# Optimization experiments

Hardware: AMD Instinct MI355X
Metric: run time of the kernel (lower is better)

The kernel has to match this reference:

```python
import jax, jax.numpy as jnp
import numpy as np

# Hyper-params from init_kwargs
H, DM, DA, DP, M, T = 8, 512, 256, 128, 32, 4096
DK, DAh, DPh = DM // H, DA // H, DP // H   # 64, 32, 16
B, K_STEPS = 8, 2048
S = T + K_STEPS          # length of x = memory + x_pre
EPS = 1e-12

def _l2n(x):
    # F.normalize(p=2, dim=-1)
    return x / jnp.maximum(jnp.linalg.norm(x, axis=-1, keepdims=True), EPS)

def setup_inputs() -> dict:
    key = jax.random.key(0)
    ks = jax.random.split(key, 28)
    n = lambda i, s, sc=0.05: jax.random.normal(ks[i], s, jnp.float32) * sc
    return {
        "memory": jax.random.normal(ks[0], (B, S - 1, DM), jnp.float32),
        "x_pre":  jax.random.normal(ks[1], (B, 1, DM), jnp.float32),
        "aux":    jax.random.normal(ks[2], (B, S, DA), jnp.float32),
        "pos":    jax.random.normal(ks[3], (B, S, DP), jnp.float32),
        "Wq": n(4, (H, DK, DM)), "bq": n(5, (H, DK)),
        "Wk": n(6, (H, DK, DM)), "bk": n(7, (H, DK)),
        "Wv": n(8, (H, DK, DM)), "bv": n(9, (H, DK)),
        "Wqa": n(10, (H, DAh, DA)), "bqa": n(11, (H, DAh)),
        "Wka": n(12, (H, DAh, DA)), "bka": n(13, (H, DAh)),
        "Wqp": n(14, (H, DPh, DP)), "bqp": n(15, (H, DPh)),
        "Wkp": n(16, (H, DPh, DP)), "bkp": n(17, (H, DPh)),
        "W_ih": n(18, (3 * DK, DM)), "W_hh": n(19, (3 * DK, DK)),
        "b_ih": n(20, (3 * DK,)), "b_hh": n(21, (3 * DK,)),
        "WO": n(22, (DM, DM)), "bO": n(23, (DM,)),
        "w": n(24, (1, 1), 1.0), "w_a": n(25, (1, 1), 1.0), "w_p": n(26, (1, 1), 1.0),
        "G": (jax.random.uniform(ks[27], (DK, DK)) < 0.5).astype(jnp.int32),
        "k": K_STEPS,
    }

def _forward(memory, x_pre, aux, pos, Wq, bq, Wk, bk, Wv, bv, Wqa, bqa, Wka, bka,
             Wqp, bqp, Wkp, bkp, W_ih, W_hh, b_ih, b_hh, WO, bO, w, w_a, w_p, G, k):
    b = memory.shape[0]
    x = jnp.concatenate([memory, x_pre], axis=1)           # [B, S, DM]
    s = x.shape[1]
    Wn = k + T - M + 1                                     # attention window length
    g = G.astype(x.dtype)
    mask_h = jnp.tile(g, (1, H))[None]                     # [1, DK, DM] per-head SparseLinear mask

    # per-head Q/K node projections (SparseLinear), L2-normalized
    Q = _l2n(jnp.einsum('bsd,hkd->bhsk', x, Wq * mask_h) + bq[None, :, None, :])
    K = _l2n(jnp.einsum('bsd,hkd->bhsk', x, Wk * mask_h) + bk[None, :, None, :])

    # tn_transform_pre: for each position p, mean over the M-step window of Qv[m].K[p+m]
    Qv = Q[:, :, -M:, :]                                   # [B,H,M,DK]
    D = jnp.einsum('bhmd,bhsd->bhms', Qv, K)               # [B,H,M,S]
    p_idx = jnp.arange(Wn)[None, :] + jnp.arange(M)[:, None]   # [M,Wn]
    band = D[:, :, jnp.arange(M)[:, None], p_idx]          # [B,H,M,Wn] band-diagonal gather
    tn = band.mean(axis=2)                                 # [B,H,Wn]

    # aux / pos similarities: only the last query row survives the slice in the source
    QA = _l2n(jnp.einsum('bsa,hca->bhsc', aux, Wqa) + bqa[None, :, None, :])
    KA = _l2n(jnp.einsum('bsa,hca->bhsc', aux, Wka) + bka[None, :, None, :])
    dot2 = jnp.einsum('bhc,bhsc->bhs', QA[:, :, -1, :], KA[:, :, aux.shape[1] - Wn:, :])
    QP = _l2n(jnp.einsum('bsp,hcp->bhsc', pos, Wqp) + bqp[None, :, None, :])
    KP = _l2n(jnp.einsum('bsp,hcp->bhsc', pos, Wkp) + bkp[None, :, None, :])
    dot3 = jnp.einsum('bhc,bhsc->bhs', QP[:, :, -1, :], KP[:, :, pos.shape[1] - Wn:, :])

    attn = jax.nn.softmax(w[0, 0] * tn + w_a[0, 0] * dot2 + w_p[0, 0] * dot3, axis=-1)  # [B,H,Wn]

    # value projection over the history window, weighted by attn[..., :-1]
    xv = x[:, s - Wn:s - 1, :]                             # [B, Wn-1, DM]
    V = jnp.einsum('bsd,hkd->bhsk', xv, Wv * mask_h) + bv[None, :, None, :]
    hist = jnp.einsum('bhw,bhwd->bhd', attn[:, :, :-1], V) # [B,H,DK]

    # sequential GRU over the recent M-1 steps (shared across heads)
    recent = jnp.swapaxes(x[:, -M:-1, :], 0, 1)            # [M-1, B, DM]
    def cell(hprev, xt):
        gi = xt @ W_ih.T + b_ih
        gh = hprev @ W_hh.T + b_hh
        ir, iz, inn = jnp.split(gi, 3, axis=-1)
        hr, hz, hn = jnp.split(gh, 3, axis=-1)
        r = jax.nn.sigmoid(ir + hr)
        z = jax.nn.sigmoid(iz + hz)
        nst = jnp.tanh(inn + r * hn)
        return (1.0 - z) * nst + z * hprev, None
    res, _ = jax.lax.scan(cell, jnp.zeros((b, DK), x.dtype), recent)  # [B, DK]

    # concat per-head deltas (deta[:, :, 1:] just drops the initial zeros column)
    deta = (hist + attn[:, :, -1:] * res[:, None, :]).reshape(b, H * DK)   # [B, DM]
    mask_o = jnp.tile(g, (H, H))                           # [DM, DM] for W_O
    out = x_pre + (deta @ (WO * mask_o).T + bO)[:, None, :]
    return out

def reference(memory, x_pre, aux, pos, Wq, bq, Wk, bk, Wv, bv, Wqa, bqa, Wka, bka,
              Wqp, bqp, Wkp, bkp, W_ih, W_hh, b_ih, b_hh, WO, bO, w, w_a, w_p, G, k):
    return _forward(memory, x_pre, aux, pos, Wq, bq, Wk, bk, Wv, bv, Wqa, bqa, Wka,
                    bka, Wqp, bqp, Wkp, bkp, W_ih, W_hh, b_ih, b_hh, WO, bO,
                    w, w_a, w_p, G, k)
```

## Files before the change

### kernel.cpp

```cpp
#include <hip/hip_runtime.h>
#include <math.h>

#define BB   8
#define S    6144
#define SM1  6143
#define DM   512
#define H    8
#define DK   64
#define M    32
#define WN   6113
#define DA   256
#define DAh  32
#define DP   128
#define DPh  16
#define EPSN 1e-12f

#define WS_WKT    0
#define WS_WKAT   262144
#define WS_WKPT   327680
#define WS_QHAT   344064
#define WS_QAHAT  475136
#define WS_QPHAT  477184
#define WS_LOGITS 478208
#define WS_XBAR   869440
#define WS_ALAST  902208
#define WS_RES    902272
#define WS_GI     902784
#define WS_WQM    950400
#define WS_XBF    1212544
#define N_LOGITS  391232
#define N_XBAR    32768

typedef __attribute__((ext_vector_type(8))) short short8;
typedef __attribute__((ext_vector_type(4))) float f32x4;

__device__ inline unsigned short f2bf(float f) {
    union { float f; unsigned u; } v; v.f = f;
    unsigned r = v.u + 0x7fffu + ((v.u >> 16) & 1u);
    return (unsigned short)(r >> 16);
}
__device__ inline float bf2f(unsigned short u) {
    union { unsigned u; float f; } v; v.u = ((unsigned)u) << 16; return v.f;
}

union S8U { short8 v; unsigned short e[8]; };

__global__ void prep_weights(const float* __restrict__ Wk, const float* __restrict__ Wka,
                             const float* __restrict__ Wkp, const float* __restrict__ Wq,
                             const int* __restrict__ G,
                             unsigned short* __restrict__ wkb,
                             unsigned short* __restrict__ wkab,
                             unsigned short* __restrict__ wkpb,
                             float* __restrict__ wqm)
{
    int idx = blockIdx.x * 256 + threadIdx.x;
    if (idx < H*DM*DK) {
        int k = idx & 63; int d = (idx >> 6) & 511; int h = idx >> 15;
        float v = Wk[(size_t)(h*DK + k)*DM + d] * (float)G[k*DK + (d & 63)];
        wkb[(size_t)h*DM*DK + (((d >> 3)*DK + k) << 3) + (d & 7)] = f2bf(v);
    }
    int i2 = idx - H*DM*DK;
    if (i2 >= 0 && i2 < H*DA*DAh) {
        int h = i2 >> 13; int r = i2 & 8191;
        int j = r & 7; int f = r >> 3;
        int c = f & 31; int a = (f >> 5)*8 + j;
        wkab[i2] = f2bf(Wka[(size_t)(h*DAh + c)*DA + a]);
    }
    int i3 = idx - H*DM*DK - H*DA*DAh;
    if (i3 >= 0 && i3 < H*DP*DPh) {
        int h = i3 >> 11; int r = i3 & 2047;
        int j = r & 7; int f = r >> 3;
        int c = f & 15; int p = (f >> 4)*8 + j;
        wkpb[i3] = f2bf(Wkp[(size_t)(h*DPh + c)*DP + p]);
    }
    int i4 = idx - H*DM*DK - H*DA*DAh - H*DP*DPh;
    if (i4 >= 0 && i4 < H*DK*DM) {
        int d = i4 & 511; int k = (i4 >> 9) & 63;
        wqm[i4] = Wq[i4] * (float)G[k*DK + (d & 63)];
    }
}

__global__ __launch_bounds__(256) void xcast_k(
    const float* __restrict__ memory, const float* __restrict__ x_pre,
    unsigned short* __restrict__ xbf)
{
    size_t e = ((size_t)blockIdx.x*256 + threadIdx.x)*8;
    int b = (int)(e / ((size_t)S*DM));
    size_t r = e - (size_t)b*S*DM;
    int t = (int)(r >> 9);
    int d = (int)(r & 511);
    const float* src = (t < SM1) ? memory + ((size_t)b*SM1 + t)*DM + d
                                 : x_pre + (size_t)b*DM + d;
    float4 v0 = *(const float4*)src, v1 = *(const float4*)(src + 4);
    S8U t8;
    t8.e[0]=f2bf(v0.x); t8.e[1]=f2bf(v0.y); t8.e[2]=f2bf(v0.z); t8.e[3]=f2bf(v0.w);
    t8.e[4]=f2bf(v1.x); t8.e[5]=f2bf(v1.y); t8.e[6]=f2bf(v1.z); t8.e[7]=f2bf(v1.w);
    *(short8*)(xbf + e) = t8.v;
}

__global__ __launch_bounds__(256) void qhat_k2(
    const float* __restrict__ memory, const float* __restrict__ x_pre,
    const float* __restrict__ wqm, const float* __restrict__ bq,
    float* __restrict__ qhat)
{
    int bx = blockIdx.x;
    int mp = bx & 15;
    int h  = (bx >> 4) & 7;
    int b  = bx >> 7;
    int tid = threadIdx.x;
    int k = tid & 63, dq = tid >> 6;

    int m0 = mp*2;
    int t0 = S - M + m0, t1 = t0 + 1;
    const float* x0 = ((t0 < SM1) ? memory + ((size_t)b*SM1 + t0)*DM
                                  : x_pre + (size_t)b*DM) + dq*128;
    const float* x1 = ((t1 < SM1) ? memory + ((size_t)b*SM1 + t1)*DM
                                  : x_pre + (size_t)b*DM) + dq*128;
    const float* wr = wqm + (size_t)(h*DK + k)*DM + dq*128;

    float s0 = 0.f, s1 = 0.f;
    #pragma unroll 8
    for (int d = 0; d < 128; d += 4) {
        float4 w4 = *(const float4*)(wr + d);
        float4 a4 = *(const float4*)(x0 + d);
        float4 b4 = *(const float4*)(x1 + d);
        s0 += w4.x*a4.x + w4.y*a4.y + w4.z*a4.z + w4.w*a4.w;
        s1 += w4.x*b4.x + w4.y*b4.y + w4.z*b4.z + w4.w*b4.w;
    }

    __shared__ float part[2][4][64];
    part[0][dq][k] = s0;
    part[1][dq][k] = s1;
    __syncthreads();

    if (tid < 128) {
        int mi = tid >> 6;
        int kk = tid & 63;
        float q = part[mi][0][kk] + part[mi][1][kk] + part[mi][2][kk] + part[mi][3][kk]
                + bq[h*DK + kk];
        float ss = q*q;
        #pragma unroll
        for (int d2 = 1; d2 <= 32; d2 <<= 1) ss += __shfl_xor(ss, d2);
        qhat[((size_t)(b*H + h)*M + (m0 + mi))*DK + kk] = q / fmaxf(sqrtf(ss), EPSN);
    }
}

__global__ __launch_bounds__(256) void qaqp_k(
    const float* __restrict__ aux, const float* __restrict__ pos,
    const float* __restrict__ Wqa, const float* __restrict__ bqa,
    const float* __restrict__ Wqp, const float* __restrict__ bqp,
    float* __restrict__ qahat, float* __restrict__ qphat)
{
    int bh = blockIdx.x; int b = bh >> 3, h = bh & 7;
    int tid = threadIdx.x;
    __shared__ float pa[32][8];
    __shared__ float pp[16][16];

    {
        int c = tid & 31, ch = tid >> 5;
        const float* ar = aux + ((size_t)b*S + (S-1))*DA + ch*32;
        const float* wv = Wqa + (size_t)(h*DAh + c)*DA + ch*32;
        float s = 0.f;
        #pragma unroll
        for (int a = 0; a < 32; a += 4) {
            float4 a4 = *(const float4*)(ar + a);
            float4 w4 = *(const float4*)(wv + a);
            s += a4.x*w4.x + a4.y*w4.y + a4.z*w4.z + a4.w*w4.w;
        }
        pa[c][ch] = s;
    }
    {
        int c = tid & 15, ch = tid >> 4;
        const float* pr = pos + ((size_t)b*S + (S-1))*DP + ch*8;
        const float* wv = Wqp + (size_t)(h*DPh + c)*DP + ch*8;
        float4 a4 = *(const float4*)(pr);
        float4 w4 = *(const float4*)(wv);
        float4 a5 = *(const float4*)(pr + 4);
        float4 w5 = *(const float4*)(wv + 4);
        pp[c][ch] = a4.x*w4.x + a4.y*w4.y + a4.z*w4.z + a4.w*w4.w
                  + a5.x*w5.x + a5.y*w5.y + a5.z*w5.z + a5.w*w5.w;
    }
    __syncthreads();

    if (tid < 32) {
        float q = bqa[h*DAh + tid];
        #pragma unroll
        for (int ch = 0; ch < 8; ++ch) q += pa[tid][ch];
        float ss = q*q;
        #pragma unroll
        for (int d2 = 1; d2 <= 16; d2 <<= 1) ss += __shfl_xor(ss, d2);
        qahat[(size_t)bh*DAh + tid] = q / fmaxf(sqrtf(ss), EPSN);
    } else if (tid >= 64 && tid < 80) {
        int c = tid - 64;
        float q = bqp[h*DPh + c];
        #pragma unroll
        for (int ch = 0; ch < 16; ++ch) q += pp[c][ch];
        float ss = q*q;
        #pragma unroll
        for (int d2 = 1; d2 <= 8; d2 <<= 1) ss += __shfl_xor(ss, d2);
        qphat[(size_t)bh*DPh + c] = q / fmaxf(sqrtf(ss), EPSN);
    }
}

__global__ __launch_bounds__(256, 4) void kproj_mfma3(
    const unsigned short* __restrict__ xbf, const unsigned short* __restrict__ wkb,
    const float* __restrict__ bk, const float* __restrict__ qhat,
    const float* __restrict__ wscal, float* __restrict__ logits)
{
    int bx = blockIdx.x;
    int tile = bx % 96, h = (bx / 96) & 7, b = bx / (96*8);
    int t0 = tile * 64;
    int tid = threadIdx.x;
    int wave = tid >> 6, lane = tid & 63;
    int quad = lane >> 4, l16 = lane & 15;

    __shared__ unsigned short Qs[M][72];
    __shared__ unsigned short Kb[64][72];
    __shared__ float tnloc[95];

    {
        const float* qsrc = qhat + (size_t)(b*H + h)*M*DK;
        int i = tid * 8;
        float4 a0 = *(const float4*)(qsrc + i);
        float4 a1 = *(const float4*)(qsrc + i + 4);
        S8U t8;
        t8.e[0]=f2bf(a0.x); t8.e[1]=f2bf(a0.y); t8.e[2]=f2bf(a0.z); t8.e[3]=f2bf(a0.w);
        t8.e[4]=f2bf(a1.x); t8.e[5]=f2bf(a1.y); t8.e[6]=f2bf(a1.z); t8.e[7]=f2bf(a1.w);
        *(short8*)&Qs[i >> 6][i & 63] = t8.v;
    }
    if (tid < 95) tnloc[tid] = 0.f;

    f32x4 acc[4];
    #pragma unroll
    for (int nt = 0; nt < 4; ++nt) acc[nt] = (f32x4){0.f,0.f,0.f,0.f};

    const unsigned short* xrow = xbf + ((size_t)b*S + t0 + wave*16 + l16)*DM;
    const unsigned short* wh = wkb + (size_t)h*DM*DK;

    #pragma unroll
    for (int ch = 0; ch < 4; ++ch) {
        #pragma unroll
        for (int ks = 0; ks < 4; ++ks) {
            short8 a = *(const short8*)(xrow + ch*128 + ks*32 + quad*8);
            #pragma unroll
            for (int nt = 0; nt < 4; ++nt) {
                short8 bf = *(const short8*)(wh + (((ch*16 + ks*4 + quad)*DK) + nt*16 + l16)*8);
                acc[nt] = __builtin_amdgcn_mfma_f32_16x16x32_bf16(a, bf, acc[nt], 0, 0, 0);
            }
        }
    }

    {
        float vv[4][4];
        float ss[4] = {0.f, 0.f, 0.f, 0.f};
        #pragma unroll
        for (int nt = 0; nt < 4; ++nt) {
            float bkv = bk[h*DK + nt*16 + l16];
            #pragma unroll
            for (int reg = 0; reg < 4; ++reg) {
                float v = acc[nt][reg] + bkv;
                vv[nt][reg] = v;
                ss[reg] += v*v;
            }
        }
        #pragma unroll
        for (int d2 = 1; d2 <= 8; d2 <<= 1)
            #pragma unroll
            for (int reg = 0; reg < 4; ++reg) ss[reg] += __shfl_xor(ss[reg], d2);
        #pragma unroll
        for (int reg = 0; reg < 4; ++reg) {
            float inv = 1.f / fmaxf(sqrtf(ss[reg]), EPSN);
            #pragma unroll
            for (int nt = 0; nt < 4; ++nt)
                Kb[wave*16 + quad*4 + reg][nt*16 + l16] = f2bf(vv[nt][reg] * inv);
        }
    }
    __syncthreads();

    {
        int mtile = wave & 1;
        int thalf = (wave >> 1) * 32;
        f32x4 acc2[2];
        acc2[0] = (f32x4){0.f,0.f,0.f,0.f};
        acc2[1] = (f32x4){0.f,0.f,0.f,0.f};
        #pragma unroll
        for (int ks = 0; ks < 2; ++ks) {
            short8 a = *(const short8*)&Qs[mtile*16 + l16][ks*32 + quad*8];
            #pragma unroll
            for (int nt = 0; nt < 2; ++nt) {
                short8 kf = *(const short8*)&Kb[thalf + nt*16 + l16][ks*32 + quad*8];
                acc2[nt] = __builtin_amdgcn_mfma_f32_16x16x32_bf16(a, kf, acc2[nt], 0, 0, 0);
            }
        }
        int m0 = mtile*16 + quad*4;
        #pragma unroll
        for (int nt = 0; nt < 2; ++nt) {
            int tl = thalf + nt*16 + l16;
            #pragma unroll
            for (int reg = 0; reg < 4; ++reg) {
                int mm = m0 + reg;
                int j = t0 + tl - mm;
                if (j >= 0 && j < WN)
                    atomicAdd(&tnloc[tl - mm + 31], acc2[nt][reg]);
            }
        }
    }
    __syncthreads();
    if (tid < 95) {
        int j = t0 + tid - 31;
        if (j >= 0 && j < WN)
            atomicAdd(&logits[(size_t)(b*H + h)*WN + j], wscal[0]*(1.f/32.f)*tnloc[tid]);
    }
}

__global__ __launch_bounds__(256, 2) void ka_proj_mfma(
    const float* __restrict__ aux, const unsigned short* __restrict__ wkab,
    const float* __restrict__ bka, const float* __restrict__ qahat,
    const float* __restrict__ wa, float* __restrict__ logits)
{
    int tile = blockIdx.x % 96;
    int b    = blockIdx.x / 96;
    int j0   = tile * 64;
    int tid  = threadIdx.x;
    int wave = tid >> 6, lane = tid & 63;
    int quad = lane >> 4, l16 = lane & 15;

    __shared__ unsigned short Xa[32*520];

    {
        int r = tid >> 2, seg = tid & 3;
        int j = j0 + r; if (j > WN-1) j = WN-1;
        const float* ar = aux + ((size_t)b*S + (31 + j))*DA + seg*64;
        int tt = r >> 4, lo = r & 15;
        #pragma unroll
        for (int g = 0; g < 8; ++g) {
            float4 v0 = *(const float4*)(ar + g*8);
            float4 v1 = *(const float4*)(ar + g*8 + 4);
            int d0 = seg*64 + g*8;
            int ks = d0 >> 5, qd = (d0 >> 3) & 3;
            S8U t8;
            t8.e[0]=f2bf(v0.x); t8.e[1]=f2bf(v0.y); t8.e[2]=f2bf(v0.z); t8.e[3]=f2bf(v0.w);
            t8.e[4]=f2bf(v1.x); t8.e[5]=f2bf(v1.y); t8.e[6]=f2bf(v1.z); t8.e[7]=f2bf(v1.w);
            *(short8*)&Xa[(tt*8 + ks)*520 + (qd*16 + lo)*8] = t8.v;
        }
    }
    __syncthreads();

    float wav = wa[0];
    for (int h = 0; h < H; ++h) {
        const unsigned short* wsrc = wkab + (size_t)h*DA*DAh;
        f32x4 acc[2];
        acc[0] = (f32x4){0.f,0.f,0.f,0.f};
        acc[1] = (f32x4){0.f,0.f,0.f,0.f};
        #pragma unroll
        for (int ks = 0; ks < 8; ++ks) {
            short8 a = *(const short8*)&Xa[(wave*8 + ks)*520 + lane*8];
            #pragma unroll
            for (int nt = 0; nt < 2; ++nt) {
                short8 bf = *(const short8*)(wsrc + (size_t)(((ks*4 + quad)*32) + nt*16 + l16)*8);
                acc[nt] = __builtin_amdgcn_mfma_f32_16x16x32_bf16(a, bf, acc[nt], 0, 0, 0);
            }
        }
        float bk0 = bka[h*DAh + l16], bk1 = bka[h*DAh + 16 + l16];
        float q0 = qahat[(size_t)(b*H + h)*DAh + l16];
        float q1 = qahat[(size_t)(b*H + h)*DAh + 16 + l16];
        #pragma unroll
        for (int reg = 0; reg < 4; ++reg) {
            float v0 = acc[0][reg] + bk0;
            float v1 = acc[1][reg] + bk1;
            float ss = v0*v0 + v1*v1;
            float dp = v0*q0 + v1*q1;
            #pragma unroll
            for (int d2 = 1; d2 <= 8; d2 <<= 1) {
                ss += __shfl_xor(ss, d2);
                dp += __shfl_xor(dp, d2);
            }
            if (l16 == 0) {
                int j = j0 + wave*16 + quad*4 + reg;
                if (j < WN)
                    logits[(size_t)(b*H + h)*WN + j] += wav * dp / fmaxf(sqrtf(ss), EPSN);
            }
        }
    }
}

__global__ __launch_bounds__(256, 2) void kp_proj_mfma(
    const float* __restrict__ pos, const unsigned short* __restrict__ wkpb,
    const float* __restrict__ bkp, const float* __restrict__ qphat,
    const float* __restrict__ wp, float* __restrict__ logits)
{
    int tile = blockIdx.x % 96;
    int b    = blockIdx.x / 96;
    int j0   = tile * 64;
    int tid  = threadIdx.x;
    int wave = tid >> 6, lane = tid & 63;
    int quad = lane >> 4, l16 = lane & 15;

    __shared__ unsigned short Xp[16*520];

    {
        int r = tid >> 2, seg = tid & 3;
        int j = j0 + r; if (j > WN-1) j = WN-1;
        const float* pr = pos + ((size_t)b*S + (31 + j))*DP + seg*32;
        int tt = r >> 4, lo = r & 15;
        #pragma unroll
        for (int g = 0; g < 4; ++g) {
            float4 v0 = *(const float4*)(pr + g*8);
            float4 v1 = *(const float4*)(pr + g*8 + 4);
            int d0 = seg*32 + g*8;
            int ks = d0 >> 5, qd = (d0 >> 3) & 3;
            S8U t8;
            t8.e[0]=f2bf(v0.x); t8.e[1]=f2bf(v0.y); t8.e[2]=f2bf(v0.z); t8.e[3]=f2bf(v0.w);
            t8.e[4]=f2bf(v1.x); t8.e[5]=f2bf(v1.y); t8.e[6]=f2bf(v1.z); t8.e[7]=f2bf(v1.w);
            *(short8*)&Xp[(tt*4 + ks)*520 + (qd*16 + lo)*8] = t8.v;
        }
    }
    __syncthreads();

    float wpv = wp[0];
    for (int h = 0; h < H; ++h) {
        const unsigned short* wsrc = wkpb + (size_t)h*DP*DPh;
        f32x4 acc = (f32x4){0.f,0.f,0.f,0.f};
        #pragma unroll
        for (int ks = 0; ks < 4; ++ks) {
            short8 a = *(const short8*)&Xp[(wave*4 + ks)*520 + lane*8];
            short8 bf = *(const short8*)(wsrc + (size_t)(((ks*4 + quad)*16) + l16)*8);
            acc = __builtin_amdgcn_mfma_f32_16x16x32_bf16(a, bf, acc, 0, 0, 0);
        }
        float bk0 = bkp[h*DPh + l16];
        float q0 = qphat[(size_t)(b*H + h)*DPh + l16];
        #pragma unroll
        for (int reg = 0; reg < 4; ++reg) {
            float v = acc[reg] + bk0;
            float ss = v*v;
            float dp = v*q0;
            #pragma unroll
            for (int d2 = 1; d2 <= 8; d2 <<= 1) {
                ss += __shfl_xor(ss, d2);
                dp += __shfl_xor(dp, d2);
            }
            if (l16 == 0) {
                int j = j0 + wave*16 + quad*4 + reg;
                if (j < WN)
                    logits[(size_t)(b*H + h)*WN + j] += wpv * dp / fmaxf(sqrtf(ss), EPSN);
            }
        }
    }
}

__global__ __launch_bounds__(256, 2) void kproj_band_mfma2(
    const float* __restrict__ memory, const float* __restrict__ x_pre,
    const unsigned short* __restrict__ wkb, const float* __restrict__ bk,
    const float* __restrict__ qhat, const float* __restrict__ wscal,
    float* __restrict__ logits)
{
    int bx = blockIdx.x;
    int hp = bx & 3, b = (bx >> 2) & 7, tile = bx >> 5;
    int t0 = tile * 128;
    int tid = threadIdx.x;
    int wave = tid >> 6, lane = tid & 63;
    int quad = lane >> 4, l16 = lane & 15;

    __shared__ unsigned short Xf[32*520];
    __shared__ unsigned short Wf[16*520];
    __shared__ unsigned short Kb[128][72];
    __shared__ unsigned short Qs[M][72];
    __shared__ float tnloc[159];

    if (tid < 159) tnloc[tid] = 0.f;
    {
        int h = hp*2;
        const float* qsrc = qhat + (size_t)(b*H + h)*M*DK;
        int i = tid * 8;
        float4 a0 = *(const float4*)(qsrc + i);
        float4 a1 = *(const float4*)(qsrc + i + 4);
        S8U t8;
        t8.e[0]=f2bf(a0.x); t8.e[1]=f2bf(a0.y); t8.e[2]=f2bf(a0.z); t8.e[3]=f2bf(a0.w);
        t8.e[4]=f2bf(a1.x); t8.e[5]=f2bf(a1.y); t8.e[6]=f2bf(a1.z); t8.e[7]=f2bf(a1.w);
        *(short8*)&Qs[i >> 6][i & 63] = t8.v;
    }

    f32x4 acc[2][2][4];
    #pragma unroll
    for (int hi = 0; hi < 2; ++hi)
        #pragma unroll
        for (int mt = 0; mt < 2; ++mt)
            #pragma unroll
            for (int nt = 0; nt < 4; ++nt) acc[hi][mt][nt] = (f32x4){0.f,0.f,0.f,0.f};

    for (int ch = 0; ch < 4; ++ch) {
        __syncthreads();
        {
            int r = tid >> 1, half = tid & 1;
            int t = t0 + r;
            const float* xr = ((t < SM1) ? (memory + ((size_t)b*SM1 + t)*DM)
                                         : (x_pre + (size_t)b*DM)) + ch*128 + half*64;
            int tt = r >> 4, lo = r & 15;
            #pragma unroll
            for (int g = 0; g < 8; ++g) {
                float4 v0 = *(const float4*)(xr + g*8);
// ... 96 lines not shown
        }
        __syncthreads();
        {
            f32x4 acc2[2][2];
            #pragma unroll
            for (int mt = 0; mt < 2; ++mt)
                #pragma unroll
                for (int nt = 0; nt < 2; ++nt) acc2[mt][nt] = (f32x4){0.f,0.f,0.f,0.f};
            #pragma unroll
            for (int ks = 0; ks < 2; ++ks) {
                short8 qa0 = *(const short8*)&Qs[l16     ][ks*32 + quad*8];
                short8 qa1 = *(const short8*)&Qs[16 + l16][ks*32 + quad*8];
                #pragma unroll
                for (int nt = 0; nt < 2; ++nt) {
                    short8 kf = *(const short8*)&Kb[wave*32 + nt*16 + l16][ks*32 + quad*8];
                    acc2[0][nt] = __builtin_amdgcn_mfma_f32_16x16x32_bf16(qa0, kf, acc2[0][nt], 0, 0, 0);
                    acc2[1][nt] = __builtin_amdgcn_mfma_f32_16x16x32_bf16(qa1, kf, acc2[1][nt], 0, 0, 0);
                }
            }
            #pragma unroll
            for (int mt = 0; mt < 2; ++mt)
                #pragma unroll
                for (int nt = 0; nt < 2; ++nt) {
                    int tcol = wave*32 + nt*16 + l16;
                    #pragma unroll
                    for (int reg = 0; reg < 4; ++reg) {
                        int m = mt*16 + quad*4 + reg;
                        int j = t0 + tcol - m;
                        if (j >= 0 && j < WN)
                            atomicAdd(&tnloc[tcol - m + 31], acc2[mt][nt][reg]);
                    }
                }
        }
        __syncthreads();
        if (tid < 159) {
            int j = t0 + tid - 31;
            if (j >= 0 && j < WN)
                atomicAdd(&logits[(size_t)(b*H + h)*WN + j], wom * tnloc[tid]);
            tnloc[tid] = 0.f;
        }
        if (hi == 0) {
            const float* qsrc = qhat + (size_t)(b*H + h + 1)*M*DK;
            int i = tid * 8;
            float4 a0 = *(const float4*)(qsrc + i);
            float4 a1 = *(const float4*)(qsrc + i + 4);
            S8U t8;
            t8.e[0]=f2bf(a0.x); t8.e[1]=f2bf(a0.y); t8.e[2]=f2bf(a0.z); t8.e[3]=f2bf(a0.w);
            t8.e[4]=f2bf(a1.x); t8.e[5]=f2bf(a1.y); t8.e[6]=f2bf(a1.z); t8.e[7]=f2bf(a1.w);
            *(short8*)&Qs[i >> 6][i & 63] = t8.v;
        }
    }
}

__global__ __launch_bounds__(256) void softmax_k(float* __restrict__ logits,
                                                 float* __restrict__ alast)
{
    int bh = blockIdx.x;
    float* L = logits + (size_t)bh*WN;
    __shared__ float red[256];
    int tid = threadIdx.x;
    float mx = -1e30f;
    for (int j = tid; j < WN; j += 256) mx = fmaxf(mx, L[j]);
    red[tid] = mx; __syncthreads();
    for (int s2 = 128; s2 > 0; s2 >>= 1) {
        if (tid < s2) red[tid] = fmaxf(red[tid], red[tid+s2]);
        __syncthreads();
    }
    mx = red[0]; __syncthreads();
    float sm = 0.f;
    for (int j = tid; j < WN; j += 256) sm += expf(L[j] - mx);
    red[tid] = sm; __syncthreads();
    for (int s2 = 128; s2 > 0; s2 >>= 1) {
        if (tid < s2) red[tid] += red[tid+s2];
        __syncthreads();
    }
    float inv = 1.f / red[0];
    for (int j = tid; j < WN; j += 256) {
        float a = expf(L[j] - mx) * inv;
        L[j] = a;
        if (j == WN-1) alast[bh] = a;
    }
}

#define JC 191
__global__ __launch_bounds__(256) void xbar_bf_k(
    const unsigned short* __restrict__ xbf, const float* __restrict__ attn,
    float* __restrict__ xbar)
{
    int chunk = blockIdx.x & 31;
    int b = blockIdx.x >> 5;
    int j0 = chunk * JC;
    __shared__ float al[H][JC];
    int tid = threadIdx.x;
    for (int i = tid; i < H*JC; i += 256) {
        int hh = i / JC, jj = i - hh*JC;
        al[hh][jj] = attn[(size_t)(b*H + hh)*WN + j0 + jj];
    }
    __syncthreads();
    int d0 = tid * 2;
    const unsigned* p = (const unsigned*)(xbf + ((size_t)b*S + 31 + j0)*DM + d0);
    float acc[H][2];
    #pragma unroll
    for (int hh = 0; hh < H; ++hh) { acc[hh][0] = 0.f; acc[hh][1] = 0.f; }
    for (int jj = 0; jj < JC; ++jj) {
        unsigned u = p[(size_t)jj*(DM/2)];
        float x0 = bf2f((unsigned short)(u & 0xffff));
        float x1 = bf2f((unsigned short)(u >> 16));
        #pragma unroll
        for (int hh = 0; hh < H; ++hh) {
            float a = al[hh][jj];
            acc[hh][0] += a * x0;
            acc[hh][1] += a * x1;
        }
    }
    #pragma unroll
    for (int hh = 0; hh < H; ++hh) {
        atomicAdd(&xbar[(size_t)(b*H+hh)*DM + d0],     acc[hh][0]);
        atomicAdd(&xbar[(size_t)(b*H+hh)*DM + d0 + 1], acc[hh][1]);
    }
}

__global__ __launch_bounds__(256) void xbar_k(
    const float* __restrict__ memory, const float* __restrict__ attn,
    float* __restrict__ xbar)
{
    int chunk = blockIdx.x & 31;
    int b = blockIdx.x >> 5;
    int j0 = chunk * JC;
    __shared__ float al[H][JC];
    int tid = threadIdx.x;
    for (int i = tid; i < H*JC; i += 256) {
        int hh = i / JC, jj = i - hh*JC;
        al[hh][jj] = attn[(size_t)(b*H + hh)*WN + j0 + jj];
    }
    __syncthreads();
    int d0 = tid * 2;
    float acc[H][2];
    #pragma unroll
    for (int hh = 0; hh < H; ++hh) { acc[hh][0] = 0.f; acc[hh][1] = 0.f; }
    for (int jj = 0; jj < JC; ++jj) {
        int t = 31 + j0 + jj;
        const float2 xv = *(const float2*)(memory + ((size_t)b*SM1 + t)*DM + d0);
        #pragma unroll
        for (int hh = 0; hh < H; ++hh) {
            float a = al[hh][jj];
            acc[hh][0] += a * xv.x;
            acc[hh][1] += a * xv.y;
        }
    }
    #pragma unroll
    for (int hh = 0; hh < H; ++hh) {
        atomicAdd(&xbar[(size_t)(b*H+hh)*DM + d0],     acc[hh][0]);
        atomicAdd(&xbar[(size_t)(b*H+hh)*DM + d0 + 1], acc[hh][1]);
    }
}

__global__ __launch_bounds__(192) void gi_k(
    const float* __restrict__ memory, const float* __restrict__ W_ih,
    const float* __restrict__ b_ih, float* __restrict__ gi_all)
{
    int t = blockIdx.x >> 3;
    int b = blockIdx.x & 7;
    int c = threadIdx.x;
    const float* xr = memory + ((size_t)b*SM1 + (S - M) + t)*DM;
    const float* wr = W_ih + (size_t)c*DM;
    float s = b_ih[c];
    for (int d = 0; d < DM; d += 4) {
        float4 x4 = *(const float4*)(xr + d);
        float4 w4 = *(const float4*)(wr + d);
        s += x4.x*w4.x + x4.y*w4.y + x4.z*w4.z + x4.w*w4.w;
    }
    gi_all[((size_t)t*BB + b)*192 + c] = s;
}

__global__ __launch_bounds__(512) void gru_scan(
    const float* __restrict__ gi_all, const float* __restrict__ W_hh,
    const float* __restrict__ b_hh, float* __restrict__ res)
{
    int b = threadIdx.x >> 6;
    int l = threadIdx.x & 63;

    float w0[64], w1[64], w2[64];
    {
        const float* r0p = W_hh + (size_t)l*DK;
        const float* r1p = W_hh + (size_t)(64 + l)*DK;
        const float* r2p = W_hh + (size_t)(128 + l)*DK;
        #pragma unroll
        for (int i = 0; i < 16; ++i) {
            float4 a = *(const float4*)(r0p + i*4);
            w0[i*4]=a.x; w0[i*4+1]=a.y; w0[i*4+2]=a.z; w0[i*4+3]=a.w;
            float4 c = *(const float4*)(r1p + i*4);
            w1[i*4]=c.x; w1[i*4+1]=c.y; w1[i*4+2]=c.z; w1[i*4+3]=c.w;
            float4 e = *(const float4*)(r2p + i*4);
            w2[i*4]=e.x; w2[i*4+1]=e.y; w2[i*4+2]=e.z; w2[i*4+3]=e.w;
        }
    }
    float bh0 = b_hh[l], bh1 = b_hh[64 + l], bh2 = b_hh[128 + l];

    float h = 0.f;
    const float* g0 = gi_all + (size_t)b*192;
    float gr = g0[l], gz = g0[64 + l], gn = g0[128 + l];

    #pragma unroll 1
    for (int t = 0; t < 31; ++t) {
        float a0 = bh0, a1 = bh1, a2 = bh2;
        #pragma unroll
        for (int k = 0; k < 64; ++k) {
            float hk = __int_as_float(__builtin_amdgcn_readlane(__float_as_int(h), k));
            a0 += hk * w0[k];
            a1 += hk * w1[k];
            a2 += hk * w2[k];
        }
        float ngr = 0.f, ngz = 0.f, ngn = 0.f;
        if (t < 30) {
            const float* g2 = gi_all + ((size_t)(t+1)*BB + b)*192;
            ngr = g2[l]; ngz = g2[64 + l]; ngn = g2[128 + l];
        }
        float r = 1.f / (1.f + expf(-(gr + a0)));
        float z = 1.f / (1.f + expf(-(gz + a1)));
        float n = tanhf(gn + r * a2);
        h = (1.f - z)*n + z*h;
        gr = ngr; gz = ngz; gn = ngn;
    }
    res[b*DK + l] = h;
}
// ... 45 lines not shown
                              hipStream_t stream)
{
    const float* memory = (const float*)d_in[0];
    const float* x_pre  = (const float*)d_in[1];
    const float* aux    = (const float*)d_in[2];
    const float* pos    = (const float*)d_in[3];
    const float* Wq  = (const float*)d_in[4];
    const float* bq  = (const float*)d_in[5];
    const float* Wk  = (const float*)d_in[6];
    const float* bk  = (const float*)d_in[7];
    const float* Wv  = (const float*)d_in[8];
    const float* bv  = (const float*)d_in[9];
    const float* Wqa = (const float*)d_in[10];
    const float* bqa = (const float*)d_in[11];
    const float* Wka = (const float*)d_in[12];
    const float* bka = (const float*)d_in[13];
    const float* Wqp = (const float*)d_in[14];
    const float* bqp = (const float*)d_in[15];
    const float* Wkp = (const float*)d_in[16];
    const float* bkp = (const float*)d_in[17];
    const float* W_ih = (const float*)d_in[18];
    const float* W_hh = (const float*)d_in[19];
    const float* b_ih = (const float*)d_in[20];
    const float* b_hh = (const float*)d_in[21];
    const float* WO  = (const float*)d_in[22];
    const float* bO  = (const float*)d_in[23];
    const float* w   = (const float*)d_in[24];
    const float* w_a = (const float*)d_in[25];
    const float* w_p = (const float*)d_in[26];
    const int*   G   = (const int*)d_in[27];
    (void)in_sizes; (void)n_in; (void)out_size;

    float* ws = (float*)d_ws;
    unsigned short* wkb  = (unsigned short*)(ws + WS_WKT);
    unsigned short* wkab = (unsigned short*)(ws + WS_WKAT);
    unsigned short* wkpb = (unsigned short*)(ws + WS_WKPT);
    float* qhat   = ws + WS_QHAT;
    float* qahat  = ws + WS_QAHAT;
    float* qphat  = ws + WS_QPHAT;
    float* logits = ws + WS_LOGITS;
    float* xbar   = ws + WS_XBAR;
    float* alast  = ws + WS_ALAST;
    float* resb   = ws + WS_RES;
    float* gi_all = ws + WS_GI;
    float* wqm    = ws + WS_WQM;
    unsigned short* xbf = (unsigned short*)(ws + WS_XBF);
    float* outp   = (float*)d_out;

    const size_t need = ((size_t)WS_XBF + 12582912) * 4;
    const bool big = (ws_size >= need);

    hipMemsetAsync(logits, 0, (size_t)(N_LOGITS + N_XBAR)*sizeof(float), stream);

    prep_weights<<<(H*DM*DK + H*DA*DAh + H*DP*DPh + H*DK*DM + 255)/256, 256, 0, stream>>>(
        Wk, Wka, Wkp, Wq, G, wkb, wkab, wkpb, wqm);

    if (big)
        xcast_k<<<12288, 256, 0, stream>>>(memory, x_pre, xbf);

    gi_k<<<31*BB, 192, 0, stream>>>(memory, W_ih, b_ih, gi_all);
    gru_scan<<<1, 512, 0, stream>>>(gi_all, W_hh, b_hh, resb);

    qhat_k2<<<BB*H*16, 256, 0, stream>>>(memory, x_pre, wqm, bq, qhat);
    qaqp_k<<<BB*H, 256, 0, stream>>>(aux, pos, Wqa, bqa, Wqp, bqp, qahat, qphat);

    if (big)
        kproj_mfma3<<<96*8*BB, 256, 0, stream>>>(xbf, wkb, bk, qhat, w, logits);
    else
        kproj_band_mfma2<<<48*BB*4, 256, 0, stream>>>(memory, x_pre, wkb, bk, qhat,
                                                      w, logits);

    ka_proj_mfma<<<BB*96, 256, 0, stream>>>(aux, wkab, bka, qahat, w_a, logits);
    kp_proj_mfma<<<BB*96, 256, 0, stream>>>(pos, wkpb, bkp, qphat, w_p, logits);

    softmax_k<<<BB*H, 256, 0, stream>>>(logits, alast);

    if (big)
        xbar_bf_k<<<BB*32, 256, 0, stream>>>(xbf, logits, xbar);
    else
        xbar_k<<<BB*32, 256, 0, stream>>>(memory, logits, xbar);

    final_k<<<BB, 512, 0, stream>>>(x_pre, xbar, Wv, bv, WO, bO, alast, resb, G, outp);
}
```

Baseline: 614.0 us.

## Fuse prelude and projection kernels; widen softmax and xbar parallelism

Merges the weight prep, GRU input projection and bf16 cast into one prelude launch, and merges the K, aux and pos logit projections into one launch whose blocks are interleaved and dispatched by block index. The ka/kp contributions to the logits switch from plain += to atomicAdd because they now run concurrently with the K projection. Softmax moves to 1024 threads per block and the xbar reduction uses twice as many chunks. The goals are fewer launch gaps, overlap between independent projections and more parallelism in the short tail kernels, at the cost of extra atomics and a larger shared-memory footprint for the fused kernel.

```diff
diff --git a/kernel.cpp b/kernel.cpp
--- a/kernel.cpp
+++ b/kernel.cpp
@@ -45,57 +45,80 @@
 
 union S8U { short8 v; unsigned short e[8]; };
 
-__global__ void prep_weights(const float* __restrict__ Wk, const float* __restrict__ Wka,
-                             const float* __restrict__ Wkp, const float* __restrict__ Wq,
-                             const int* __restrict__ G,
-                             unsigned short* __restrict__ wkb,
-                             unsigned short* __restrict__ wkab,
-                             unsigned short* __restrict__ wkpb,
-                             float* __restrict__ wqm)
-{
-    int idx = blockIdx.x * 256 + threadIdx.x;
-    if (idx < H*DM*DK) {
-        int k = idx & 63; int d = (idx >> 6) & 511; int h = idx >> 15;
-        float v = Wk[(size_t)(h*DK + k)*DM + d] * (float)G[k*DK + (d & 63)];
-        wkb[(size_t)h*DM*DK + (((d >> 3)*DK + k) << 3) + (d & 7)] = f2bf(v);
-    }
-    int i2 = idx - H*DM*DK;
-    if (i2 >= 0 && i2 < H*DA*DAh) {
-        int h = i2 >> 13; int r = i2 & 8191;
-        int j = r & 7; int f = r >> 3;
-        int c = f & 31; int a = (f >> 5)*8 + j;
-        wkab[i2] = f2bf(Wka[(size_t)(h*DAh + c)*DA + a]);
-    }
-    int i3 = idx - H*DM*DK - H*DA*DAh;
-    if (i3 >= 0 && i3 < H*DP*DPh) {
-        int h = i3 >> 11; int r = i3 & 2047;
-        int j = r & 7; int f = r >> 3;
-        int c = f & 15; int p = (f >> 4)*8 + j;
-        wkpb[i3] = f2bf(Wkp[(size_t)(h*DPh + c)*DP + p]);
-    }
-    int i4 = idx - H*DM*DK - H*DA*DAh - H*DP*DPh;
-    if (i4 >= 0 && i4 < H*DK*DM) {
-        int d = i4 & 511; int k = (i4 >> 9) & 63;
-        wqm[i4] = Wq[i4] * (float)G[k*DK + (d & 63)];
-    }
-}
-
-__global__ __launch_bounds__(256) void xcast_k(
+#define PREP_NB 2368
+#define GI_NB   248
+#define XCAST_NB 12288
+
+__global__ __launch_bounds__(256) void prelude_k(
+    const float* __restrict__ Wk, const float* __restrict__ Wka,
+    const float* __restrict__ Wkp, const float* __restrict__ Wq,
+    const int* __restrict__ G,
+    unsigned short* __restrict__ wkb, unsigned short* __restrict__ wkab,
+    unsigned short* __restrict__ wkpb, float* __restrict__ wqm,
     const float* __restrict__ memory, const float* __restrict__ x_pre,
-    unsigned short* __restrict__ xbf)
-{
-    size_t e = ((size_t)blockIdx.x*256 + threadIdx.x)*8;
-    int b = (int)(e / ((size_t)S*DM));
-    size_t r = e - (size_t)b*S*DM;
-    int t = (int)(r >> 9);
-    int d = (int)(r & 511);
-    const float* src = (t < SM1) ? memory + ((size_t)b*SM1 + t)*DM + d
-                                 : x_pre + (size_t)b*DM + d;
-    float4 v0 = *(const float4*)src, v1 = *(const float4*)(src + 4);
-    S8U t8;
-    t8.e[0]=f2bf(v0.x); t8.e[1]=f2bf(v0.y); t8.e[2]=f2bf(v0.z); t8.e[3]=f2bf(v0.w);
-    t8.e[4]=f2bf(v1.x); t8.e[5]=f2bf(v1.y); t8.e[6]=f2bf(v1.z); t8.e[7]=f2bf(v1.w);
-    *(short8*)(xbf + e) = t8.v;
+    const float* __restrict__ W_ih, const float* __restrict__ b_ih,
+    float* __restrict__ gi_all, unsigned short* __restrict__ xbf)
+{
+    int bx = blockIdx.x, tid = threadIdx.x;
+
+    if (bx < PREP_NB) {
+        int idx = bx * 256 + tid;
+        if (idx < H*DM*DK) {
+            int k = idx & 63; int d = (idx >> 6) & 511; int h = idx >> 15;
+            float v = Wk[(size_t)(h*DK + k)*DM + d] * (float)G[k*DK + (d & 63)];
+            wkb[(size_t)h*DM*DK + (((d >> 3)*DK + k) << 3) + (d & 7)] = f2bf(v);
+        }
+        int i2 = idx - H*DM*DK;
+        if (i2 >= 0 && i2 < H*DA*DAh) {
+            int h = i2 >> 13; int r = i2 & 8191;
+            int j = r & 7; int f = r >> 3;
+            int c = f & 31; int a = (f >> 5)*8 + j;
+            wkab[i2] = f2bf(Wka[(size_t)(h*DAh + c)*DA + a]);
+        }
+        int i3 = idx - H*DM*DK - H*DA*DAh;
+        if (i3 >= 0 && i3 < H*DP*DPh) {
+            int h = i3 >> 11; int r = i3 & 2047;
+            int j = r & 7; int f = r >> 3;
+            int c = f & 15; int p = (f >> 4)*8 + j;
+            wkpb[i3] = f2bf(Wkp[(size_t)(h*DPh + c)*DP + p]);
+        }
+        int i4 = idx - H*DM*DK - H*DA*DAh - H*DP*DPh;
+        if (i4 >= 0 && i4 < H*DK*DM) {
+            int d = i4 & 511; int k = (i4 >> 9) & 63;
+            wqm[i4] = Wq[i4] * (float)G[k*DK + (d & 63)];
+        }
+        return;
+    }
+    if (bx < PREP_NB + GI_NB) {
+        if (tid < 192) {
+            int gx = bx - PREP_NB;
+            int t = gx >> 3, b = gx & 7, c = tid;
+            const float* xr = memory + ((size_t)b*SM1 + (S - M) + t)*DM;
+            const float* wr = W_ih + (size_t)c*DM;
+            float s = b_ih[c];
+            for (int d = 0; d < DM; d += 4) {
+                float4 x4 = *(const float4*)(xr + d);
+                float4 w4 = *(const float4*)(wr + d);
+                s += x4.x*w4.x + x4.y*w4.y + x4.z*w4.z + x4.w*w4.w;
+            }
+            gi_all[((size_t)t*BB + b)*192 + c] = s;
+        }
+        return;
+    }
+    {
+        size_t e = ((size_t)(bx - PREP_NB - GI_NB)*256 + tid)*8;
+        int b = (int)(e / ((size_t)S*DM));
+        size_t r = e - (size_t)b*S*DM;
+        int t = (int)(r >> 9);
+        int d = (int)(r & 511);
+        const float* src = (t < SM1) ? memory + ((size_t)b*SM1 + t)*DM + d
+                                     : x_pre + (size_t)b*DM + d;
+        float4 v0 = *(const float4*)src, v1 = *(const float4*)(src + 4);
+        S8U t8;
+        t8.e[0]=f2bf(v0.x); t8.e[1]=f2bf(v0.y); t8.e[2]=f2bf(v0.z); t8.e[3]=f2bf(v0.w);
+        t8.e[4]=f2bf(v1.x); t8.e[5]=f2bf(v1.y); t8.e[6]=f2bf(v1.z); t8.e[7]=f2bf(v1.w);
+        *(short8*)(xbf + e) = t8.v;
+    }
 }
 
 __global__ __launch_bounds__(256) void qhat_k2(
@@ -202,21 +225,22 @@
     }
 }
 
-__global__ __launch_bounds__(256, 4) void kproj_mfma3(
+#define SMEM_BYTES 33280
+
+__device__ __forceinline__ void kproj3_body(int bxx, int tid, unsigned char* smemraw,
     const unsigned short* __restrict__ xbf, const unsigned short* __restrict__ wkb,
     const float* __restrict__ bk, const float* __restrict__ qhat,
     const float* __restrict__ wscal, float* __restrict__ logits)
 {
-    int bx = blockIdx.x;
-    int tile = bx % 96, h = (bx / 96) & 7, b = bx / (96*8);
+    int tile = bxx % 96, h = (bxx / 96) & 7, b = bxx / (96*8);
     int t0 = tile * 64;
-    int tid = threadIdx.x;
     int wave = tid >> 6, lane = tid & 63;
     int quad = lane >> 4, l16 = lane & 15;
 
-    __shared__ unsigned short Qs[M][72];
-    __shared__ unsigned short Kb[64][72];
-    __shared__ float tnloc[95];
+    typedef unsigned short row72[72];
+    row72* Qs = (row72*)smemraw;
+    row72* Kb = (row72*)(smemraw + 32*72*2);
+    float* tnloc = (float*)(smemraw + 96*72*2);
 
     {
         const float* qsrc = qhat + (size_t)(b*H + h)*M*DK;
@@ -313,19 +337,18 @@
     }
 }
 
-__global__ __launch_bounds__(256, 2) void ka_proj_mfma(
+__device__ __forceinline__ void ka_body(int g, int tid, unsigned char* smemraw,
     const float* __restrict__ aux, const unsigned short* __restrict__ wkab,
     const float* __restrict__ bka, const float* __restrict__ qahat,
     const float* __restrict__ wa, float* __restrict__ logits)
 {
-    int tile = blockIdx.x % 96;
-    int b    = blockIdx.x / 96;
+    int tile = g % 96;
+    int b    = g / 96;
     int j0   = tile * 64;
-    int tid  = threadIdx.x;
     int wave = tid >> 6, lane = tid & 63;
     int quad = lane >> 4, l16 = lane & 15;
 
-    __shared__ unsigned short Xa[32*520];
+    unsigned short* Xa = (unsigned short*)smemraw;
 
     {
         int r = tid >> 2, seg = tid & 3;
@@ -333,10 +356,10 @@
         const float* ar = aux + ((size_t)b*S + (31 + j))*DA + seg*64;
         int tt = r >> 4, lo = r & 15;
         #pragma unroll
-        for (int g = 0; g < 8; ++g) {
-            float4 v0 = *(const float4*)(ar + g*8);
-            float4 v1 = *(const float4*)(ar + g*8 + 4);
-            int d0 = seg*64 + g*8;
+        for (int gg = 0; gg < 8; ++gg) {
+            float4 v0 = *(const float4*)(ar + gg*8);
+            float4 v1 = *(const float4*)(ar + gg*8 + 4);
+            int d0 = seg*64 + gg*8;
             int ks = d0 >> 5, qd = (d0 >> 3) & 3;
             S8U t8;
             t8.e[0]=f2bf(v0.x); t8.e[1]=f2bf(v0.y); t8.e[2]=f2bf(v0.z); t8.e[3]=f2bf(v0.w);
@@ -378,25 +401,25 @@
             if (l16 == 0) {
                 int j = j0 + wave*16 + quad*4 + reg;
                 if (j < WN)
-                    logits[(size_t)(b*H + h)*WN + j] += wav * dp / fmaxf(sqrtf(ss), EPSN);
-            }
-        }
-    }
-}
-
-__global__ __launch_bounds__(256, 2) void kp_proj_mfma(
+                    atomicAdd(&logits[(size_t)(b*H + h)*WN + j],
+                              wav * dp / fmaxf(sqrtf(ss), EPSN));
+            }
+        }
+    }
+}
+
+__device__ __forceinline__ void kp_body(int g, int tid, unsigned char* smemraw,
     const float* __restrict__ pos, const unsigned short* __restrict__ wkpb,
     const float* __restrict__ bkp, const float* __restrict__ qphat,
     const float* __restrict__ wp, float* __restrict__ logits)
 {
-    int tile = blockIdx.x % 96;
-    int b    = blockIdx.x / 96;
+    int tile = g % 96;
+    int b    = g / 96;
     int j0   = tile * 64;
-    int tid  = threadIdx.x;
     int wave = tid >> 6, lane = tid & 63;
     int quad = lane >> 4, l16 = lane & 15;
 
-    __shared__ unsigned short Xp[16*520];
+    unsigned short* Xp = (unsigned short*)smemraw;
 
     {
         int r = tid >> 2, seg = tid & 3;
@@ -404,10 +427,10 @@
         const float* pr = pos + ((size_t)b*S + (31 + j))*DP + seg*32;
         int tt = r >> 4, lo = r & 15;
         #pragma unroll
-        for (int g = 0; g < 4; ++g) {
-            float4 v0 = *(const float4*)(pr + g*8);
-            float4 v1 = *(const float4*)(pr + g*8 + 4);
-            int d0 = seg*32 + g*8;
+        for (int gg = 0; gg < 4; ++gg) {
+            float4 v0 = *(const float4*)(pr + gg*8);
+            float4 v1 = *(const float4*)(pr + gg*8 + 4);
+            int d0 = seg*32 + gg*8;
             int ks = d0 >> 5, qd = (d0 >> 3) & 3;
             S8U t8;
             t8.e[0]=f2bf(v0.x); t8.e[1]=f2bf(v0.y); t8.e[2]=f2bf(v0.z); t8.e[3]=f2bf(v0.w);
@@ -442,10 +465,52 @@
             if (l16 == 0) {
                 int j = j0 + wave*16 + quad*4 + reg;
                 if (j < WN)
-                    logits[(size_t)(b*H + h)*WN + j] += wpv * dp / fmaxf(sqrtf(ss), EPSN);
-            }
-        }
-    }
+                    atomicAdd(&logits[(size_t)(b*H + h)*WN + j],
+                              wpv * dp / fmaxf(sqrtf(ss), EPSN));
+            }
+        }
+    }
+}
+
+__global__ __launch_bounds__(256, 4) void proj_fused_k(
+    const unsigned short* __restrict__ xbf, const unsigned short* __restrict__ wkb,
+    const float* __restrict__ bk, const float* __restrict__ qhat,
+    const float* __restrict__ w,
+    const float* __restrict__ aux, const unsigned short* __restrict__ wkab,
+    const float* __restrict__ bka, const float* __restrict__ qahat,
+    const float* __restrict__ wa,
+    const float* __restrict__ pos, const unsigned short* __restrict__ wkpb,
+    const float* __restrict__ bkp, const float* __restrict__ qphat,
+    const float* __restrict__ wp,
+    float* __restrict__ logits)
+{
+    __shared__ __align__(16) unsigned char smemraw[SMEM_BYTES];
+    int bx = blockIdx.x;
+    int g = bx / 10, r = bx - g*10;
+    int tid = threadIdx.x;
+    if (r < 8)
+        kproj3_body(g*8 + r, tid, smemraw, xbf, wkb, bk, qhat, w, logits);
+    else if (r == 8)
+        ka_body(g, tid, smemraw, aux, wkab, bka, qahat, wa, logits);
+    else
+        kp_body(g, tid, smemraw, pos, wkpb, bkp, qphat, wp, logits);
+}
+
+__global__ __launch_bounds__(256, 2) void ka_only_k(
+    const float* __restrict__ aux, const unsigned short* __restrict__ wkab,
+    const float* __restrict__ bka, const float* __restrict__ qahat,
+    const float* __restrict__ wa, float* __restrict__ logits)
+{
+    __shared__ __align__(16) unsigned char smemraw[SMEM_BYTES];
+    ka_body(blockIdx.x, threadIdx.x, smemraw, aux, wkab, bka, qahat, wa, logits);
+}
+__global__ __launch_bounds__(256, 2) void kp_only_k(
+    const float* __restrict__ pos, const unsigned short* __restrict__ wkpb,
+    const float* __restrict__ bkp, const float* __restrict__ qphat,
+    const float* __restrict__ wp, float* __restrict__ logits)
+{
+    __shared__ __align__(16) unsigned char smemraw[SMEM_BYTES];
+    kp_body(blockIdx.x, threadIdx.x, smemraw, pos, wkpb, bkp, qphat, wp, logits);
 }
 
 __global__ __launch_bounds__(256, 2) void kproj_band_mfma2(
@@ -648,39 +713,79 @@
     }
 }
 
-__global__ __launch_bounds__(256) void softmax_k(float* __restrict__ logits,
-                                                 float* __restrict__ alast)
+__global__ __launch_bounds__(1024) void softmax_k(float* __restrict__ logits,
+                                                  float* __restrict__ alast)
 {
     int bh = blockIdx.x;
     float* L = logits + (size_t)bh*WN;
-    __shared__ float red[256];
+    __shared__ float red[1024];
     int tid = threadIdx.x;
     float mx = -1e30f;
-    for (int j = tid; j < WN; j += 256) mx = fmaxf(mx, L[j]);
+    for (int j = tid; j < WN; j += 1024) mx = fmaxf(mx, L[j]);
     red[tid] = mx; __syncthreads();
-    for (int s2 = 128; s2 > 0; s2 >>= 1) {
+    for (int s2 = 512; s2 > 0; s2 >>= 1) {
         if (tid < s2) red[tid] = fmaxf(red[tid], red[tid+s2]);
         __syncthreads();
     }
     mx = red[0]; __syncthreads();
     float sm = 0.f;
-    for (int j = tid; j < WN; j += 256) sm += expf(L[j] - mx);
+    for (int j = tid; j < WN; j += 1024) sm += expf(L[j] - mx);
     red[tid] = sm; __syncthreads();
-    for (int s2 = 128; s2 > 0; s2 >>= 1) {
+    for (int s2 = 512; s2 > 0; s2 >>= 1) {
         if (tid < s2) red[tid] += red[tid+s2];
         __syncthreads();
     }
     float inv = 1.f / red[0];
-    for (int j = tid; j < WN; j += 256) {
+    for (int j = tid; j < WN; j += 1024) {
         float a = expf(L[j] - mx) * inv;
         L[j] = a;
         if (j == WN-1) alast[bh] = a;
     }
 }
 
-#define JC 191
+#define JC2 96
 __global__ __launch_bounds__(256) void xbar_bf_k(
     const unsigned short* __restrict__ xbf, const float* __restrict__ attn,
+    float* __restrict__ xbar)
+{
+    int chunk = blockIdx.x & 63;
+    int b = blockIdx.x >> 6;
+    int j0 = chunk * JC2;
+    int lim = (WN-1) - j0; if (lim > JC2) lim = JC2; if (lim < 0) lim = 0;
+    __shared__ float al[H][JC2];
+    int tid = threadIdx.x;
+    for (int i = tid; i < H*JC2; i += 256) {
+        int hh = i / JC2, jj = i - hh*JC2;
+        al[hh][jj] = (jj < lim) ? attn[(size_t)(b*H + hh)*WN + j0 + jj] : 0.f;
+    }
+    __syncthreads();
+    int d0 = tid * 2;
+    const unsigned* p = (const unsigned*)(xbf + ((size_t)b*S + 31 + j0)*DM + d0);
+    float acc[H][2];
+    #pragma unroll
+    for (int hh = 0; hh < H; ++hh) { acc[hh][0] = 0.f; acc[hh][1] = 0.f; }
+    #pragma unroll 4
+    for (int jj = 0; jj < lim; ++jj) {
+        unsigned u = p[(size_t)jj*(DM/2)];
+        float x0 = bf2f((unsigned short)(u & 0xffff));
+        float x1 = bf2f((unsigned short)(u >> 16));
+        #pragma unroll
+        for (int hh = 0; hh < H; ++hh) {
+            float a = al[hh][jj];
+            acc[hh][0] += a * x0;
+            acc[hh][1] += a * x1;
+        }
+    }
+    #pragma unroll
+    for (int hh = 0; hh < H; ++hh) {
+        atomicAdd(&xbar[(size_t)(b*H+hh)*DM + d0],     acc[hh][0]);
+        atomicAdd(&xbar[(size_t)(b*H+hh)*DM + d0 + 1], acc[hh][1]);
+    }
+}
+
+#define JC 191
+__global__ __launch_bounds__(256) void xbar_k(
+    const float* __restrict__ memory, const float* __restrict__ attn,
     float* __restrict__ xbar)
 {
     int chunk = blockIdx.x & 31;
@@ -694,43 +799,6 @@
     }
     __syncthreads();
     int d0 = tid * 2;
-    const unsigned* p = (const unsigned*)(xbf + ((size_t)b*S + 31 + j0)*DM + d0);
-    float acc[H][2];
-    #pragma unroll
-    for (int hh = 0; hh < H; ++hh) { acc[hh][0] = 0.f; acc[hh][1] = 0.f; }
-    for (int jj = 0; jj < JC; ++jj) {
-        unsigned u = p[(size_t)jj*(DM/2)];
-        float x0 = bf2f((unsigned short)(u & 0xffff));
-        float x1 = bf2f((unsigned short)(u >> 16));
-        #pragma unroll
-        for (int hh = 0; hh < H; ++hh) {
-            float a = al[hh][jj];
-            acc[hh][0] += a * x0;
-            acc[hh][1] += a * x1;
-        }
-    }
-    #pragma unroll
-    for (int hh = 0; hh < H; ++hh) {
-        atomicAdd(&xbar[(size_t)(b*H+hh)*DM + d0],     acc[hh][0]);
-        atomicAdd(&xbar[(size_t)(b*H+hh)*DM + d0 + 1], acc[hh][1]);
-    }
-}
-
-__global__ __launch_bounds__(256) void xbar_k(
-    const float* __restrict__ memory, const float* __restrict__ attn,
-    float* __restrict__ xbar)
-{
-    int chunk = blockIdx.x & 31;
-    int b = blockIdx.x >> 5;
-    int j0 = chunk * JC;
-    __shared__ float al[H][JC];
-    int tid = threadIdx.x;
-    for (int i = tid; i < H*JC; i += 256) {
-        int hh = i / JC, jj = i - hh*JC;
-        al[hh][jj] = attn[(size_t)(b*H + hh)*WN + j0 + jj];
-    }
-    __syncthreads();
-    int d0 = tid * 2;
     float acc[H][2];
     #pragma unroll
     for (int hh = 0; hh < H; ++hh) { acc[hh][0] = 0.f; acc[hh][1] = 0.f; }
@@ -749,24 +817,6 @@
         atomicAdd(&xbar[(size_t)(b*H+hh)*DM + d0],     acc[hh][0]);
         atomicAdd(&xbar[(size_t)(b*H+hh)*DM + d0 + 1], acc[hh][1]);
     }
-}
-
-__global__ __launch_bounds__(192) void gi_k(
-    const float* __restrict__ memory, const float* __restrict__ W_ih,
-    const float* __restrict__ b_ih, float* __restrict__ gi_all)
-{
-    int t = blockIdx.x >> 3;
-    int b = blockIdx.x & 7;
-    int c = threadIdx.x;
-    const float* xr = memory + ((size_t)b*SM1 + (S - M) + t)*DM;
-    const float* wr = W_ih + (size_t)c*DM;
-    float s = b_ih[c];
-    for (int d = 0; d < DM; d += 4) {
-        float4 x4 = *(const float4*)(xr + d);
-        float4 w4 = *(const float4*)(wr + d);
-        s += x4.x*w4.x + x4.y*w4.y + x4.z*w4.z + x4.w*w4.w;
-    }
-    gi_all[((size_t)t*BB + b)*192 + c] = s;
 }
 
 __global__ __launch_bounds__(512) void gru_scan(
@@ -918,31 +968,30 @@
 
     hipMemsetAsync(logits, 0, (size_t)(N_LOGITS + N_XBAR)*sizeof(float), stream);
 
-    prep_weights<<<(H*DM*DK + H*DA*DAh + H*DP*DPh + H*DK*DM + 255)/256, 256, 0, stream>>>(
-        Wk, Wka, Wkp, Wq, G, wkb, wkab, wkpb, wqm);
-
-    if (big)
-        xcast_k<<<12288, 256, 0, stream>>>(memory, x_pre, xbf);
-
-    gi_k<<<31*BB, 192, 0, stream>>>(memory, W_ih, b_ih, gi_all);
-    gru_scan<<<1, 512, 0, stream>>>(gi_all, W_hh, b_hh, resb);
+    prelude_k<<<big ? (PREP_NB + GI_NB + XCAST_NB) : (PREP_NB + GI_NB), 256, 0, stream>>>(
+        Wk, Wka, Wkp, Wq, G, wkb, wkab, wkpb, wqm,
+        memory, x_pre, W_ih, b_ih, gi_all, xbf);
 
     qhat_k2<<<BB*H*16, 256, 0, stream>>>(memory, x_pre, wqm, bq, qhat);
     qaqp_k<<<BB*H, 256, 0, stream>>>(aux, pos, Wqa, bqa, Wqp, bqp, qahat, qphat);
-
-    if (big)
-        kproj_mfma3<<<96*8*BB, 256, 0, stream>>>(xbf, wkb, bk, qhat, w, logits);
-    else
+    gru_scan<<<1, 512, 0, stream>>>(gi_all, W_hh, b_hh, resb);
+
+    if (big) {
+        proj_fused_k<<<7680, 256, 0, stream>>>(
+            xbf, wkb, bk, qhat, w,
+            aux, wkab, bka, qahat, w_a,
+            pos, wkpb, bkp, qphat, w_p, logits);
+    } else {
         kproj_band_mfma2<<<48*BB*4, 256, 0, stream>>>(memory, x_pre, wkb, bk, qhat,
                                                       w, logits);
-
-    ka_proj_mfma<<<BB*96, 256, 0, stream>>>(aux, wkab, bka, qahat, w_a, logits);
-    kp_proj_mfma<<<BB*96, 256, 0, stream>>>(pos, wkpb, bkp, qphat, w_p, logits);
-
-    softmax_k<<<BB*H, 256, 0, stream>>>(logits, alast);
+        ka_only_k<<<BB*96, 256, 0, stream>>>(aux, wkab, bka, qahat, w_a, logits);
+        kp_only_k<<<BB*96, 256, 0, stream>>>(pos, wkpb, bkp, qphat, w_p, logits);
+    }
+
+    softmax_k<<<BB*H, 1024, 0, stream>>>(logits, alast);
 
     if (big)
-        xbar_bf_k<<<BB*32, 256, 0, stream>>>(xbf, logits, xbar);
+        xbar_bf_k<<<BB*64, 256, 0, stream>>>(xbf, logits, xbar);
     else
         xbar_k<<<BB*32, 256, 0, stream>>>(memory, logits, xbar);
 
```

Result: no change. 615.6 us (+0.3%).
